# Optimization experiments

Hardware: AMD Instinct MI355X
Metric: run time of the kernel (lower is better)

Reference implementation:

```python
import jax, jax.numpy as jnp
import numpy as np
import math

D, H, L, V, F, B, S = 1024, 16, 4, 32000, 4096, 1, 2048
HD = D // H
LN_EPS = 1e-5


def _alibi_slopes(n_heads):
    # power-of-2 case from the torch code
    start = 2.0 ** (-2.0 ** (-(math.log2(n_heads) - 3)))
    return np.array([start * (start ** i) for i in range(n_heads)], dtype=np.float32)


def setup_inputs() -> dict:
    key = jax.random.key(0)
    ks = jax.random.split(key, 10)
    sc = 0.02
    return {
        "input_ids": jax.random.randint(ks[0], (B, S), 0, V, dtype=jnp.int64 if jax.config.jax_enable_x64 else jnp.int32),
        "emb": jax.random.normal(ks[1], (V, D), jnp.float32) * sc,
        "alibi_slopes": jnp.asarray(_alibi_slopes(H)),
        "Wq": jax.random.normal(ks[2], (L, D, D), jnp.float32) * sc,
        "Wk": jax.random.normal(ks[3], (L, D, D), jnp.float32) * sc,
        "Wv": jax.random.normal(ks[4], (L, D, D), jnp.float32) * sc,
        "Wo": jax.random.normal(ks[5], (L, D, D), jnp.float32) * sc,
        "W1": jax.random.normal(ks[6], (L, F, D), jnp.float32) * sc,
        "b1": jnp.zeros((L, F), jnp.float32),
        "W2": jax.random.normal(ks[7], (L, D, F), jnp.float32) * sc,
        "b2": jnp.zeros((L, D), jnp.float32),
        "g1": jnp.ones((L, D), jnp.float32),
        "beta1": jnp.zeros((L, D), jnp.float32),
        "g2": jnp.ones((L, D), jnp.float32),
        "beta2": jnp.zeros((L, D), jnp.float32),
        "gf": jnp.ones((D,), jnp.float32),
        "bf": jnp.zeros((D,), jnp.float32),
    }


def _layernorm(x, g, b):
    m = jnp.mean(x, axis=-1, keepdims=True)
    v = jnp.var(x, axis=-1, keepdims=True)
    return (x - m) * jax.lax.rsqrt(v + LN_EPS) * g + b


def _forward(input_ids, emb, alibi_slopes, Wq, Wk, Wv, Wo, W1, b1, W2, b2,
             g1, beta1, g2, beta2, gf, bf):
    x = emb[input_ids]  # [B, S, D]
    pos = jnp.arange(S, dtype=jnp.float32)
    dist = pos[None, :] - pos[:, None]          # [S, S], entry (i, j) = j - i
    causal = dist <= 0                           # tril mask
    bias = alibi_slopes[None, :, None, None] * dist  # [1, H, S, S]
    scale = 1.0 / math.sqrt(HD)

    def layer(x, p):
        wq, wk, wv, wo, w1, bb1, w2, bb2, gg1, be1, gg2, be2 = p
        h = _layernorm(x, gg1, be1)
        q = jnp.einsum('bsd,ed->bse', h, wq).reshape(B, S, H, HD).transpose(0, 2, 1, 3)
        k = jnp.einsum('bsd,ed->bse', h, wk).reshape(B, S, H, HD).transpose(0, 2, 1, 3)
        v = jnp.einsum('bsd,ed->bse', h, wv).reshape(B, S, H, HD).transpose(0, 2, 1, 3)
        scores = jnp.einsum('bhqd,bhkd->bhqk', q, k) * scale
        scores = scores - bias
        scores = jnp.where(causal, scores, -jnp.inf)
        w = jax.nn.softmax(scores, axis=-1)
        out = jnp.einsum('bhqk,bhkd->bhqd', w, v)
        out = out.transpose(0, 2, 1, 3).reshape(B, S, D)
        out = jnp.einsum('bsd,ed->bse', out, wo)
        x = x + out
        h2 = _layernorm(x, gg2, be2)
        ff = jax.nn.gelu(jnp.einsum('bsd,fd->bsf', h2, w1) + bb1, approximate=False)
        ff = jnp.einsum('bsf,df->bsd', ff, w2) + bb2
        return x + ff, None

    params = (Wq, Wk, Wv, Wo, W1, b1, W2, b2, g1, beta1, g2, beta2)
    x, _ = jax.lax.scan(layer, x, params)
    x = _layernorm(x, gf, bf)
    logits = jnp.einsum('bsd,vd->bsv', x, emb)  # tied lm_head
    return logits


def reference(input_ids, emb, alibi_slopes, Wq, Wk, Wv, Wo, W1, b1, W2, b2,
              g1, beta1, g2, beta2, gf, bf):
    return _forward(input_ids, emb, alibi_slopes, Wq, Wk, Wv, Wo, W1, b1, W2, b2,
                    g1, beta1, g2, beta2, gf, bf)
```

## Files before the change

### kernel.cpp

```cpp
#include <hip/hip_runtime.h>
#include <hip/hip_bf16.h>

typedef unsigned int u32;
typedef unsigned short u16;
typedef __attribute__((ext_vector_type(8))) __bf16 bf16x8;
typedef __attribute__((ext_vector_type(8))) unsigned short u16x8;
typedef __attribute__((ext_vector_type(4))) float f32x4;

#define SEQ 2048

__device__ __forceinline__ float b2f(u16 u) {
  union { u32 i; float f; } x; x.i = ((u32)u) << 16; return x.f;
}
__device__ __forceinline__ u16 f2b(float f) {
  u32 u = __float_as_uint(f);
  u = (u + 0x7fffu + ((u >> 16) & 1u)) >> 16;
  return (u16)u;
}
__device__ __forceinline__ void gload_lds16(const void* g, void* l) {
  __builtin_amdgcn_global_load_lds((const __attribute__((address_space(1))) u32*)g,
                                   (__attribute__((address_space(3))) u32*)l, 16, 0, 0);
}

struct CvtArgs {
  const float* src[7];
  u16* dst[7];
  u32 beg[8];
  u32 total;
};

__global__ __launch_bounds__(256) void cvt_all(CvtArgs a)
{
  for (u32 i = blockIdx.x * 256 + threadIdx.x; i < a.total; i += gridDim.x * 256) {
    int s = 0;
#pragma unroll
    for (int k = 1; k < 7; ++k) s += (i >= a.beg[k]);
    const u32 li = i - a.beg[s];
    const float* in = a.src[s];
    const float4 f0 = ((const float4*)in)[(size_t)li * 2];
    const float4 f1 = ((const float4*)in)[(size_t)li * 2 + 1];
    union { bf16x8 b; u16x8 u; } r;
    r.b[0] = (__bf16)f0.x; r.b[1] = (__bf16)f0.y;
    r.b[2] = (__bf16)f0.z; r.b[3] = (__bf16)f0.w;
    r.b[4] = (__bf16)f1.x; r.b[5] = (__bf16)f1.y;
    r.b[6] = (__bf16)f1.z; r.b[7] = (__bf16)f1.w;
    *(u16x8*)(a.dst[s] + (size_t)li * 8) = r.u;
  }
}

__global__ __launch_bounds__(512, 2) void gemm256(
    const u16* __restrict__ A, const u16* __restrict__ Bt,
    float* __restrict__ C, int N, int K)
{
  __shared__ u16 As[2][256 * 64];
  __shared__ u16 Bs[2][256 * 64];
  const int tid = threadIdx.x;
  const int lane = tid & 63;
  const int wid = tid >> 6;
  const int wr = wid >> 2;
  const int wc = wid & 3;

  const int T = (int)gridDim.x;
  const int bid = (int)blockIdx.x;
  const int q8 = T >> 3, r8 = T & 7;
  const int xcd = bid & 7, base = bid >> 3;
  const int swz = (xcd < r8 ? xcd * (q8 + 1) : r8 * (q8 + 1) + (xcd - r8) * q8) + base;
  const int m0 = (swz & 7) * 256;
  const int n0 = (swz >> 3) * 256;

  f32x4 acc[8][4] = {};

  const int srow = tid >> 3;
  const int sgr = (tid & 7) ^ (srow & 7);
  const u16* gA = A + (size_t)(m0 + srow) * K + sgr * 8;
  const u16* gB = Bt + (size_t)(n0 + srow) * K + sgr * 8;
  const int dwave = wid * 512;

  const int co0 = (((lane >> 4)) ^ (lane & 7)) * 8;
  const int co1 = (((lane >> 4) + 4) ^ (lane & 7)) * 8;
  const int raA = (wr * 128 + (lane & 15)) * 64;
  const int raB = (wc * 64 + (lane & 15)) * 64;

  const int nk = K >> 6;

#pragma unroll
  for (int c = 0; c < 4; ++c) {
    gload_lds16(gA + (size_t)(c * 64) * K, &As[0][c * 4096 + dwave]);
    gload_lds16(gB + (size_t)(c * 64) * K, &Bs[0][c * 4096 + dwave]);
  }
#pragma unroll
  for (int c = 0; c < 4; ++c) {
    gload_lds16(gA + (size_t)(c * 64) * K + 64, &As[1][c * 4096 + dwave]);
    gload_lds16(gB + (size_t)(c * 64) * K + 64, &Bs[1][c * 4096 + dwave]);
  }
  asm volatile("s_waitcnt vmcnt(8)" ::: "memory");
  __builtin_amdgcn_s_barrier();
  __builtin_amdgcn_sched_barrier(0);

#pragma unroll 2
  for (int t = 0; t < nk; ++t) {
    const int cb = t & 1;
    const u16* Acur = &As[cb][0];
    const u16* Bcur = &Bs[cb][0];

    bf16x8 bf[4][2];
#pragma unroll
    for (int n = 0; n < 4; ++n) {
      const int ro = raB + n * 16 * 64;
      bf[n][0] = *(const bf16x8*)&Bcur[ro + co0];
      bf[n][1] = *(const bf16x8*)&Bcur[ro + co1];
    }
#pragma unroll
    for (int p = 0; p < 4; ++p) {
      bf16x8 af[2][2];
#pragma unroll
      for (int mm = 0; mm < 2; ++mm) {
        const int ro = raA + (p * 32 + mm * 16) * 64;
        af[mm][0] = *(const bf16x8*)&Acur[ro + co0];
        af[mm][1] = *(const bf16x8*)&Acur[ro + co1];
      }
      __builtin_amdgcn_s_setprio(1);
#pragma unroll
      for (int mm = 0; mm < 2; ++mm)
#pragma unroll
        for (int n = 0; n < 4; ++n) {
          acc[p * 2 + mm][n] = __builtin_amdgcn_mfma_f32_16x16x32_bf16(af[mm][0], bf[n][0], acc[p * 2 + mm][n], 0, 0, 0);
          acc[p * 2 + mm][n] = __builtin_amdgcn_mfma_f32_16x16x32_bf16(af[mm][1], bf[n][1], acc[p * 2 + mm][n], 0, 0, 0);
        }
      __builtin_amdgcn_s_setprio(0);
    }

    __builtin_amdgcn_s_barrier();
    if (t + 2 < nk) {
      const size_t kto = (size_t)(t + 2) * 64;
      u16* Anx = &As[cb][0];
      u16* Bnx = &Bs[cb][0];
#pragma unroll
      for (int c = 0; c < 4; ++c) {
        gload_lds16(gA + (size_t)(c * 64) * K + kto, Anx + c * 4096 + dwave);
        gload_lds16(gB + (size_t)(c * 64) * K + kto, Bnx + c * 4096 + dwave);
      }
      asm volatile("s_waitcnt vmcnt(8)" ::: "memory");
    } else if (t + 1 < nk) {
      asm volatile("s_waitcnt vmcnt(0)" ::: "memory");
    }
    __builtin_amdgcn_s_barrier();
    __builtin_amdgcn_sched_barrier(0);
  }

  const int crow = m0 + wr * 128 + ((lane >> 4) << 2);
  const int ccol = n0 + wc * 64 + (lane & 15);
#pragma unroll
  for (int m = 0; m < 8; ++m)
#pragma unroll
    for (int n = 0; n < 4; ++n)
#pragma unroll
      for (int j = 0; j < 4; ++j)
        C[(size_t)(crow + m * 16 + j) * N + ccol + n * 16] = acc[m][n][j];
}

template <int EPI>
__global__ __launch_bounds__(256) void gemm64(
    const u16* __restrict__ A, const u16* __restrict__ B0,
    const u16* __restrict__ B1, const u16* __restrict__ B2,
    void* __restrict__ C0, void* __restrict__ C1, void* __restrict__ C2,
    const float* __restrict__ bias, int N, int K)
{
  __shared__ u16 As[64 * 64];
  __shared__ u16 Bs[128 * 64];
  const int tid = threadIdx.x;
  const int lane = tid & 63;
  const int w = tid >> 6;
  const int wr = w >> 1;
  const int wc = w & 1;

  const int T = (int)gridDim.x;
  const int bid = (int)blockIdx.x;
  const int q8 = T >> 3, r8 = T & 7;
  const int xcd = bid & 7, base = bid >> 3;
  int swz = (xcd < r8 ? xcd * (q8 + 1) : r8 * (q8 + 1) + (xcd - r8) * q8) + base;
  int which = 0;
  if (EPI == 1) which = swz >> 8;
  const u16* Bt = (which == 0) ? B0 : (which == 1) ? B1 : B2;
  const int m0 = (swz & 31) * 64;
  const int n0 = (EPI == 1 ? ((swz >> 5) & 7) : (swz >> 5)) * 128;

  const int kchunk = K / (int)gridDim.z;
  const int kbeg = (int)blockIdx.z * kchunk;
  const int kend = kbeg + kchunk;

  f32x4 acc[2][4] = {};

  const int rs = lane >> 3;
  const int gs = (lane & 7) ^ rs;
  const u16* ga0 = A + (size_t)(m0 + w * 16 + rs) * K + gs * 8;
  const u16* gb0 = Bt + (size_t)(n0 + w * 32 + rs) * K + gs * 8;
  u16* la = &As[(w * 16) * 64];
  u16* lb = &Bs[(w * 32) * 64];

  const int xg = lane & 7;
  int coff[2];
#pragma unroll
  for (int ks = 0; ks < 2; ++ks)
    coff[ks] = ((ks * 4 + (lane >> 4)) ^ xg) * 8;
  const int ra = (wr * 32 + (lane & 15)) * 64;
  const int rb = (wc * 64 + (lane & 15)) * 64;

  for (int kt = kbeg; kt < kend; kt += 64) {
    __syncthreads();
#pragma unroll
    for (int c = 0; c < 2; ++c)
      gload_lds16(ga0 + (size_t)c * 8 * K + kt, la + c * 8 * 64);
#pragma unroll
    for (int c = 0; c < 4; ++c)
      gload_lds16(gb0 + (size_t)c * 8 * K + kt, lb + c * 8 * 64);
    asm volatile("s_waitcnt vmcnt(0)" ::: "memory");
    __syncthreads();
#pragma unroll
    for (int ks = 0; ks < 2; ++ks) {
      bf16x8 af[2], bfr[4];
#pragma unroll
      for (int m = 0; m < 2; ++m)
        af[m] = *(const bf16x8*)&As[ra + m * 16 * 64 + coff[ks]];
#pragma unroll
      for (int n = 0; n < 4; ++n)
        bfr[n] = *(const bf16x8*)&Bs[rb + n * 16 * 64 + coff[ks]];
#pragma unroll
      for (int m = 0; m < 2; ++m)
#pragma unroll
        for (int n = 0; n < 4; ++n)
          acc[m][n] = __builtin_amdgcn_mfma_f32_16x16x32_bf16(af[m], bfr[n], acc[m][n], 0, 0, 0);
    }
  }

#pragma unroll
  for (int m = 0; m < 2; ++m) {
    const int rowb = m0 + wr * 32 + m * 16 + ((lane >> 4) << 2);
#pragma unroll
    for (int n = 0; n < 4; ++n) {
      const int col = n0 + wc * 64 + n * 16 + (lane & 15);
#pragma unroll
      for (int j = 0; j < 4; ++j) {
        const int r = rowb + j;
        float v = acc[m][n][j];
        if (EPI == 1) {
          u16* outp = (u16*)((which == 0) ? C0 : (which == 1) ? C1 : C2);
          outp[((size_t)(col >> 6) * SEQ + r) * 64 + (col & 63)] = f2b(v);
        } else if (EPI == 2) {
          float xx = v + bias[col];
          float ge = 0.5f * xx * (1.0f + erff(xx * 0.70710678118654752f));
          ((u16*)C0)[(size_t)r * N + col] = f2b(ge);
        } else {
          float xx = v;
          if (bias != nullptr && blockIdx.z == 0) xx += bias[col];
          atomicAdd(&((float*)C0)[(size_t)r * N + col], xx);
        }
      }
    }
  }
}

__global__ __launch_bounds__(256) void gemm_f32b(
    const u16* __restrict__ A, const float* __restrict__ Bt,
    float* __restrict__ C0, int N, int K)
{
  __shared__ u16 As[128 * 32];
  __shared__ u16 Bs[128 * 32];
  const int tid = threadIdx.x;
  const int lane = tid & 63;
  const int w = tid >> 6;
  const int wr = w >> 1;
  const int wc = w & 1;

  const int T = (int)gridDim.x;
  const int bid = (int)blockIdx.x;
  const int q8 = T >> 3, r8 = T & 7;
  const int xcd = bid & 7, base = bid >> 3;
  int swz = (xcd < r8 ? xcd * (q8 + 1) : r8 * (q8 + 1) + (xcd - r8) * q8) + base;
  const int m0 = (swz & 15) * 128;
  const int n0 = (swz >> 4) * 128;

  f32x4 acc[4][4] = {};
  const u16* ga0 = A + (size_t)(m0 + w * 32 + (lane >> 2)) * K + (lane & 3) * 8;
  u16* la = &As[(w * 32) * 32];
  const float* gb32 = Bt + (size_t)(n0 + (tid >> 1)) * K + (tid & 1) * 16;
  u16* lbw = &Bs[(tid >> 1) * 32 + (tid & 1) * 16];

  for (int kt = 0; kt < K; kt += 32) {
    __syncthreads();
    gload_lds16(ga0 + kt, la);
    gload_lds16(ga0 + kt + 16 * K, la + 16 * 32);
    {
      const float4 f0 = *(const float4*)(gb32 + kt);
      const float4 f1 = *(const float4*)(gb32 + kt + 4);
      const float4 f2 = *(const float4*)(gb32 + kt + 8);
      const float4 f3 = *(const float4*)(gb32 + kt + 12);
      union { bf16x8 b; u16x8 u; } lo, hi;
      lo.b[0] = (__bf16)f0.x; lo.b[1] = (__bf16)f0.y;
      lo.b[2] = (__bf16)f0.z; lo.b[3] = (__bf16)f0.w;
      lo.b[4] = (__bf16)f1.x; lo.b[5] = (__bf16)f1.y;
      lo.b[6] = (__bf16)f1.z; lo.b[7] = (__bf16)f1.w;
      hi.b[0] = (__bf16)f2.x; hi.b[1] = (__bf16)f2.y;
      hi.b[2] = (__bf16)f2.z; hi.b[3] = (__bf16)f2.w;
      hi.b[4] = (__bf16)f3.x; hi.b[5] = (__bf16)f3.y;
      hi.b[6] = (__bf16)f3.z; hi.b[7] = (__bf16)f3.w;
      *(u16x8*)lbw = lo.u;
      *(u16x8*)(lbw + 8) = hi.u;
    }
    asm volatile("s_waitcnt vmcnt(0)" ::: "memory");
    __syncthreads();
    bf16x8 af[4], bfr[4];
#pragma unroll
    for (int m = 0; m < 4; ++m)
      af[m] = *(const bf16x8*)&As[(wr * 64 + m * 16 + (lane & 15)) * 32 + (lane >> 4) * 8];
#pragma unroll
    for (int n = 0; n < 4; ++n)
      bfr[n] = *(const bf16x8*)&Bs[(wc * 64 + n * 16 + (lane & 15)) * 32 + (lane >> 4) * 8];
#pragma unroll
    for (int m = 0; m < 4; ++m)
#pragma unroll
      for (int n = 0; n < 4; ++n)
        acc[m][n] = __builtin_amdgcn_mfma_f32_16x16x32_bf16(af[m], bfr[n], acc[m][n], 0, 0, 0);
  }

#pragma unroll
  for (int m = 0; m < 4; ++m) {
    const int rowb = m0 + wr * 64 + m * 16 + ((lane >> 4) << 2);
#pragma unroll
    for (int n = 0; n < 4; ++n) {
      const int col = n0 + wc * 64 + n * 16 + (lane & 15);
#pragma unroll
      for (int j = 0; j < 4; ++j)
        C0[(size_t)(rowb + j) * N + col] = acc[m][n][j];
    }
  }
}

__global__ __launch_bounds__(256) void ln_kernel(const float* __restrict__ x,
    const float* __restrict__ g, const float* __restrict__ b, u16* __restrict__ out)
{
  const int row = blockIdx.x;
  const int tid = threadIdx.x;
  const float4 v = ((const float4*)(x + (size_t)row * 1024))[tid];
  float s = v.x + v.y + v.z + v.w;
  float sq = v.x * v.x + v.y * v.y + v.z * v.z + v.w * v.w;
#pragma unroll
  for (int o = 1; o < 64; o <<= 1) { s += __shfl_xor(s, o); sq += __shfl_xor(sq, o); }
  __shared__ float ss[4], ssq[4];
  if ((tid & 63) == 0) { ss[tid >> 6] = s; ssq[tid >> 6] = sq; }
  __syncthreads();
  s = ss[0] + ss[1] + ss[2] + ss[3];
  sq = ssq[0] + ssq[1] + ssq[2] + ssq[3];
  const float mean = s * (1.0f / 1024.0f);
  const float var = sq * (1.0f / 1024.0f) - mean * mean;
  const float rstd = rsqrtf(var + 1e-5f);
  const int c = tid * 4;
  u16* o4 = out + (size_t)row * 1024 + c;
  const float4 gg = ((const float4*)g)[tid];
  const float4 bb = ((const float4*)b)[tid];
  o4[0] = f2b((v.x - mean) * rstd * gg.x + bb.x);
  o4[1] = f2b((v.y - mean) * rstd * gg.y + bb.y);
  o4[2] = f2b((v.z - mean) * rstd * gg.z + bb.z);
  o4[3] = f2b((v.w - mean) * rstd * gg.w + bb.w);
}

__global__ __launch_bounds__(256) void gather_kernel(const int* __restrict__ ids,
    const float* __restrict__ emb, float* __restrict__ x)
{
  const int srow = blockIdx.x;
  const int tid = threadIdx.x;
  const int id = ids[srow];
  ((float4*)(x + (size_t)srow * 1024))[tid] =
      ((const float4*)(emb + (size_t)id * 1024))[tid];
}

__global__ __launch_bounds__(256) void attn_kernel(
    const u16* __restrict__ q, const u16* __restrict__ k, const u16* __restrict__ v,
    const float* __restrict__ slopes, u16* __restrict__ out)
{
  const int bid = (int)blockIdx.x;
  const int swz = (bid & 7) * 32 + (bid >> 3);
  const int h = swz >> 4;
  const int q0 = (swz & 15) * 128;
  const int tid = threadIdx.x;
  const int lane = tid & 63;
  const int w = tid >> 6;
  const float slope = slopes[h];

  __shared__ u16 Ks[2][64 * 32];
  __shared__ u16 Vt[64][72];
  __shared__ u16 Pl[4][32][72];

  const u16* qb = q + ((size_t)h * SEQ + q0 + w * 32) * 64;
  bf16x8 qf[2][2];
#pragma unroll
  for (int m = 0; m < 2; ++m)
#pragma unroll
    for (int kk = 0; kk < 2; ++kk)
      qf[m][kk] = *(const bf16x8*)(qb + (m * 16 + (lane & 15)) * 64 + kk * 32 + (lane >> 4) * 8);

  f32x4 o_acc[2][4] = {};
  float mrun[2][4], lrun[2][4];
#pragma unroll
  for (int m = 0; m < 2; ++m)
#pragma unroll
    for (int j = 0; j < 4; ++j) { mrun[m][j] = -1e30f; lrun[m][j] = 0.0f; }

  const int ntiles = (q0 >> 6) + 2;
  const int wmaxrow = q0 + w * 32 + 31;

  const int kkp = w >> 1, halfp = w & 1;
  const u16* gk0 = k + ((size_t)h * SEQ + halfp * 32 + (lane >> 2)) * 64 + kkp * 32 + (lane & 3) * 8;
  u16* lk = &Ks[kkp][(halfp * 32) * 32];
  const u16* gv0 = v + ((size_t)h * SEQ + lane) * 64 + w * 16;

  for (int t = 0; t < ntiles; ++t) {
    const int j0 = t << 6;
    __syncthreads();
    gload_lds16(gk0 + (size_t)j0 * 64, lk);
    gload_lds16(gk0 + (size_t)(j0 + 16) * 64, lk + 16 * 32);
    {
      const u16* gvp = gv0 + (size_t)j0 * 64;
      u16x8 v0 = *(const u16x8*)gvp;
      u16x8 v1 = *(const u16x8*)(gvp + 8);
      const int d0 = w * 16;
#pragma unroll
      for (int i = 0; i < 8; ++i) Vt[d0 + i][lane] = v0[i];
#pragma unroll
      for (int i = 0; i < 8; ++i) Vt[d0 + 8 + i][lane] = v1[i];
    }
    asm volatile("s_waitcnt vmcnt(0)" ::: "memory");
    __syncthreads();

    if (wmaxrow >= j0) {
      f32x4 s[2][4] = {};
      __builtin_amdgcn_s_setprio(1);
#pragma unroll
      for (int kk = 0; kk < 2; ++kk) {
        bf16x8 kf[4];
#pragma unroll
        for (int n = 0; n < 4; ++n)
          kf[n] = *(const bf16x8*)&Ks[kk][(n * 16 + (lane & 15)) * 32 + (lane >> 4) * 8];
#pragma unroll
        for (int m = 0; m < 2; ++m)
#pragma unroll
          for (int n = 0; n < 4; ++n)
            s[m][n] = __builtin_amdgcn_mfma_f32_16x16x32_bf16(qf[m][kk], kf[n], s[m][n], 0, 0, 0);
      }
      __builtin_amdgcn_s_setprio(0);
      const int rq = q0 + w * 32 + ((lane >> 4) << 2);
      const int ck = j0 + (lane & 15);
#pragma unroll
      for (int m = 0; m < 2; ++m) {
#pragma unroll
        for (int j = 0; j < 4; ++j) {
          const int qi = rq + m * 16 + j;
          float mx = -1e30f;
#pragma unroll
          for (int n = 0; n < 4; ++n) {
            const int kj = ck + n * 16;
            float val = s[m][n][j] * 0.125f - slope * (float)(kj - qi);
            val = (kj <= qi) ? val : -1e30f;
            s[m][n][j] = val;
            mx = fmaxf(mx, val);
          }
#pragma unroll
          for (int o = 1; o < 16; o <<= 1) mx = fmaxf(mx, __shfl_xor(mx, o));
          const float mnew = fmaxf(mrun[m][j], mx);
          const float alpha = __expf(mrun[m][j] - mnew);
          mrun[m][j] = mnew;
          float rs = 0.0f;
          const int prow = m * 16 + ((lane >> 4) << 2) + j;
#pragma unroll
          for (int n = 0; n < 4; ++n) {
            const float p = __expf(s[m][n][j] - mnew);
            rs += p;
            Pl[w][prow][n * 16 + (lane & 15)] = f2b(p);
          }
#pragma unroll
          for (int o = 1; o < 16; o <<= 1) rs += __shfl_xor(rs, o);
          lrun[m][j] = lrun[m][j] * alpha + rs;
#pragma unroll
          for (int n = 0; n < 4; ++n) o_acc[m][n][j] *= alpha;
        }
      }
      __builtin_amdgcn_s_setprio(1);
#pragma unroll
      for (int kk = 0; kk < 2; ++kk) {
        bf16x8 pf[2], vf[4];
#pragma unroll
        for (int m = 0; m < 2; ++m)
          pf[m] = *(const bf16x8*)&Pl[w][m * 16 + (lane & 15)][kk * 32 + (lane >> 4) * 8];
#pragma unroll
        for (int n = 0; n < 4; ++n)
          vf[n] = *(const bf16x8*)&Vt[n * 16 + (lane & 15)][kk * 32 + (lane >> 4) * 8];
#pragma unroll
        for (int m = 0; m < 2; ++m)
#pragma unroll
          for (int n = 0; n < 4; ++n)
            o_acc[m][n] = __builtin_amdgcn_mfma_f32_16x16x32_bf16(pf[m], vf[n], o_acc[m][n], 0, 0, 0);
      }
      __builtin_amdgcn_s_setprio(0);
    }
  }

#pragma unroll
  for (int m = 0; m < 2; ++m) {
    const int sbase = q0 + w * 32 + m * 16 + ((lane >> 4) << 2);
#pragma unroll
    for (int n = 0; n < 4; ++n) {
      const int d = h * 64 + n * 16 + (lane & 15);
#pragma unroll
      for (int j = 0; j < 4; ++j)
        out[(size_t)(sbase + j) * 1024 + d] = f2b(o_acc[m][n][j] / lrun[m][j]);
    }
  }
}

extern "C" void kernel_launch(void* const* d_in, const int* in_sizes, int n_in,
                              void* d_out, int out_size, void* d_ws, size_t ws_size,
                              hipStream_t stream)
{
  (void)in_sizes; (void)n_in; (void)out_size;
  const int* ids = (const int*)d_in[0];
  const float* emb = (const float*)d_in[1];
  const float* slopes = (const float*)d_in[2];
  const float* Wq = (const float*)d_in[3];
  const float* Wk = (const float*)d_in[4];
  const float* Wv = (const float*)d_in[5];
  const float* Wo = (const float*)d_in[6];
  const float* W1 = (const float*)d_in[7];
  const float* b1 = (const float*)d_in[8];
  const float* W2 = (const float*)d_in[9];
  const float* b2 = (const float*)d_in[10];
  const float* g1 = (const float*)d_in[11];
  const float* be1 = (const float*)d_in[12];
  const float* g2 = (const float*)d_in[13];
  const float* be2 = (const float*)d_in[14];
  const float* gf = (const float*)d_in[15];
  const float* bfin = (const float*)d_in[16];

  char* ob = (char*)d_out;
  float* x   = (float*)ob;
  u16* qb    = (u16*)(ob + (size_t)( 8u << 20));
  u16* kb    = (u16*)(ob + (size_t)(12u << 20));
  u16* vb    = (u16*)(ob + (size_t)(16u << 20));
  u16* attn  = (u16*)(ob + (size_t)(20u << 20));
  u16* ff    = (u16*)(ob + (size_t)(24u << 20));
  u16* Wq_b  = (u16*)(ob + (size_t)( 40u << 20));
  u16* Wk_b  = (u16*)(ob + (size_t)( 48u << 20));
  u16* Wv_b  = (u16*)(ob + (size_t)( 56u << 20));
  u16* Wo_b  = (u16*)(ob + (size_t)( 64u << 20));
  u16* W1_b  = (u16*)(ob + (size_t)( 72u << 20));
  u16* W2_b  = (u16*)(ob + (size_t)(104u << 20));
  u16* h     = (u16*)d_ws;
  const size_t emb_b_need = (size_t)(4u << 20) + (size_t)32000 * 1024 * 2;
  const bool emb_fits = ws_size >= emb_b_need;
  u16* emb_b = (u16*)((char*)d_ws + (4u << 20));
  float* logits = (float*)d_out;

  {
    CvtArgs a;
    const u32 wsz = 4 * 1024 * 1024 / 8;
    const u32 fsz = 16 * 1024 * 1024 / 8;
    const u32 esz = 32000 * 1024 / 8;
    a.src[0] = Wq; a.dst[0] = Wq_b;
    a.src[1] = Wk; a.dst[1] = Wk_b;
    a.src[2] = Wv; a.dst[2] = Wv_b;
    a.src[3] = Wo; a.dst[3] = Wo_b;
    a.src[4] = W1; a.dst[4] = W1_b;
    a.src[5] = W2; a.dst[5] = W2_b;
    a.src[6] = emb; a.dst[6] = emb_b;
    a.beg[0] = 0;
    a.beg[1] = wsz;      a.beg[2] = 2 * wsz;  a.beg[3] = 3 * wsz;
    a.beg[4] = 4 * wsz;  a.beg[5] = 4 * wsz + fsz;  a.beg[6] = 4 * wsz + 2 * fsz;
    a.beg[7] = a.beg[6] + esz;
    a.total = emb_fits ? a.beg[7] : a.beg[6];
    cvt_all<<<2048, 256, 0, stream>>>(a);
  }

  gather_kernel<<<2048, 256, 0, stream>>>(ids, emb, x);

  for (int l = 0; l < 4; ++l) {
    const size_t wo = (size_t)l * 1024 * 1024;
    const size_t wf = (size_t)l * 4096 * 1024;
    ln_kernel<<<2048, 256, 0, stream>>>(x, g1 + l * 1024, be1 + l * 1024, h);
    gemm64<1><<<dim3(768, 1, 1), 256, 0, stream>>>(h, Wq_b + wo, Wk_b + wo, Wv_b + wo,
        qb, kb, vb, nullptr, 1024, 1024);
    attn_kernel<<<dim3(256, 1, 1), 256, 0, stream>>>(qb, kb, vb, slopes, attn);
    gemm64<3><<<dim3(256, 1, 2), 256, 0, stream>>>(attn, Wo_b + wo, nullptr, nullptr,
        x, nullptr, nullptr, nullptr, 1024, 1024);
    ln_kernel<<<2048, 256, 0, stream>>>(x, g2 + l * 1024, be2 + l * 1024, h);
    gemm64<2><<<dim3(1024, 1, 1), 256, 0, stream>>>(h, W1_b + wf, nullptr, nullptr,
        ff, nullptr, nullptr, b1 + l * 4096, 4096, 1024);
    gemm64<3><<<dim3(256, 1, 2), 256, 0, stream>>>(ff, W2_b + wf, nullptr, nullptr,
        x, nullptr, nullptr, b2 + l * 1024, 1024, 4096);
  }
  ln_kernel<<<2048, 256, 0, stream>>>(x, gf, bfin, h);
  if (emb_fits) {
    gemm256<<<dim3(1000, 1, 1), 512, 0, stream>>>(h, emb_b, logits, 32000, 1024);
  } else {
    gemm_f32b<<<dim3(4000, 1, 1), 256, 0, stream>>>(h, emb, logits, 32000, 1024);
  }
}
```

Measured before the change: 1.319 ms.

## Replace gemm64 with double-buffered 128x128 GEMM, fuse QKV weights and residual+LN

Replaces the single-buffered 64x128 GEMM with a 128x128 tile kernel that double-buffers LDS loads and raises MFMA priority. The Q/K/V weights are interleaved per layer at conversion time so one N=3072 GEMM produces all three projections. Split-K partial sums now go to two fp32 scratch buffers instead of atomics, and a new ln_res kernel adds residual, partials and bias and then applies the next LayerNorm. This removes the atomics and the separate LN launches, at the cost of extra scratch traffic and fewer blocks for the N=1024 GEMMs.

```diff
diff --git a/kernel.cpp b/kernel.cpp
--- a/kernel.cpp
+++ b/kernel.cpp
@@ -44,7 +44,15 @@
     r.b[2] = (__bf16)f0.z; r.b[3] = (__bf16)f0.w;
     r.b[4] = (__bf16)f1.x; r.b[5] = (__bf16)f1.y;
     r.b[6] = (__bf16)f1.z; r.b[7] = (__bf16)f1.w;
-    *(u16x8*)(a.dst[s] + (size_t)li * 8) = r.u;
+    u16* d;
+    if (s < 3) {
+      const u32 layer = li >> 17;
+      const u32 rem = li & 131071u;
+      d = a.dst[s] + ((size_t)layer * 393216u + rem) * 8;
+    } else {
+      d = a.dst[s] + (size_t)li * 8;
+    }
+    *(u16x8*)d = r.u;
   }
 }
 
@@ -160,82 +168,110 @@
 }
 
 template <int EPI>
-__global__ __launch_bounds__(256) void gemm64(
-    const u16* __restrict__ A, const u16* __restrict__ B0,
-    const u16* __restrict__ B1, const u16* __restrict__ B2,
+__global__ __launch_bounds__(256, 2) void gemm128p(
+    const u16* __restrict__ A, const u16* __restrict__ Bt,
     void* __restrict__ C0, void* __restrict__ C1, void* __restrict__ C2,
     const float* __restrict__ bias, int N, int K)
 {
-  __shared__ u16 As[64 * 64];
-  __shared__ u16 Bs[128 * 64];
+  __shared__ u16 As[2][128 * 64];
+  __shared__ u16 Bs[2][128 * 64];
   const int tid = threadIdx.x;
   const int lane = tid & 63;
-  const int w = tid >> 6;
-  const int wr = w >> 1;
-  const int wc = w & 1;
+  const int wid = tid >> 6;
+  const int wr = wid >> 1;
+  const int wc = wid & 1;
 
   const int T = (int)gridDim.x;
   const int bid = (int)blockIdx.x;
   const int q8 = T >> 3, r8 = T & 7;
   const int xcd = bid & 7, base = bid >> 3;
-  int swz = (xcd < r8 ? xcd * (q8 + 1) : r8 * (q8 + 1) + (xcd - r8) * q8) + base;
-  int which = 0;
-  if (EPI == 1) which = swz >> 8;
-  const u16* Bt = (which == 0) ? B0 : (which == 1) ? B1 : B2;
-  const int m0 = (swz & 31) * 64;
-  const int n0 = (EPI == 1 ? ((swz >> 5) & 7) : (swz >> 5)) * 128;
+  const int swz = (xcd < r8 ? xcd * (q8 + 1) : r8 * (q8 + 1) + (xcd - r8) * q8) + base;
+  const int m0 = (swz & 15) * 128;
+  const int n0 = (swz >> 4) * 128;
 
   const int kchunk = K / (int)gridDim.z;
   const int kbeg = (int)blockIdx.z * kchunk;
-  const int kend = kbeg + kchunk;
-
-  f32x4 acc[2][4] = {};
-
-  const int rs = lane >> 3;
-  const int gs = (lane & 7) ^ rs;
-  const u16* ga0 = A + (size_t)(m0 + w * 16 + rs) * K + gs * 8;
-  const u16* gb0 = Bt + (size_t)(n0 + w * 32 + rs) * K + gs * 8;
-  u16* la = &As[(w * 16) * 64];
-  u16* lb = &Bs[(w * 32) * 64];
-
-  const int xg = lane & 7;
-  int coff[2];
-#pragma unroll
-  for (int ks = 0; ks < 2; ++ks)
-    coff[ks] = ((ks * 4 + (lane >> 4)) ^ xg) * 8;
-  const int ra = (wr * 32 + (lane & 15)) * 64;
-  const int rb = (wc * 64 + (lane & 15)) * 64;
-
-  for (int kt = kbeg; kt < kend; kt += 64) {
-    __syncthreads();
-#pragma unroll
-    for (int c = 0; c < 2; ++c)
-      gload_lds16(ga0 + (size_t)c * 8 * K + kt, la + c * 8 * 64);
-#pragma unroll
-    for (int c = 0; c < 4; ++c)
-      gload_lds16(gb0 + (size_t)c * 8 * K + kt, lb + c * 8 * 64);
-    asm volatile("s_waitcnt vmcnt(0)" ::: "memory");
-    __syncthreads();
-#pragma unroll
-    for (int ks = 0; ks < 2; ++ks) {
-      bf16x8 af[2], bfr[4];
-#pragma unroll
-      for (int m = 0; m < 2; ++m)
-        af[m] = *(const bf16x8*)&As[ra + m * 16 * 64 + coff[ks]];
-#pragma unroll
-      for (int n = 0; n < 4; ++n)
-        bfr[n] = *(const bf16x8*)&Bs[rb + n * 16 * 64 + coff[ks]];
-#pragma unroll
-      for (int m = 0; m < 2; ++m)
-#pragma unroll
-        for (int n = 0; n < 4; ++n)
-          acc[m][n] = __builtin_amdgcn_mfma_f32_16x16x32_bf16(af[m], bfr[n], acc[m][n], 0, 0, 0);
-    }
-  }
-
-#pragma unroll
-  for (int m = 0; m < 2; ++m) {
-    const int rowb = m0 + wr * 32 + m * 16 + ((lane >> 4) << 2);
+  const int nk = kchunk >> 6;
+
+  f32x4 acc[4][4] = {};
+
+  const int srow = tid >> 3;
+  const int sgr = (tid & 7) ^ (srow & 7);
+  const u16* gA = A + (size_t)(m0 + srow) * K + kbeg + sgr * 8;
+  const u16* gB = Bt + (size_t)(n0 + srow) * K + kbeg + sgr * 8;
+  const int dwave = wid * 512;
+
+  const int co0 = (((lane >> 4)) ^ (lane & 7)) * 8;
+  const int co1 = (((lane >> 4) + 4) ^ (lane & 7)) * 8;
+  const int raA = (wr * 64 + (lane & 15)) * 64;
+  const int raB = (wc * 64 + (lane & 15)) * 64;
+
+#pragma unroll
+  for (int c = 0; c < 4; ++c) {
+    gload_lds16(gA + (size_t)(c * 32) * K, &As[0][c * 2048 + dwave]);
+    gload_lds16(gB + (size_t)(c * 32) * K, &Bs[0][c * 2048 + dwave]);
+  }
+#pragma unroll
+  for (int c = 0; c < 4; ++c) {
+    gload_lds16(gA + (size_t)(c * 32) * K + 64, &As[1][c * 2048 + dwave]);
+    gload_lds16(gB + (size_t)(c * 32) * K + 64, &Bs[1][c * 2048 + dwave]);
+  }
+  asm volatile("s_waitcnt vmcnt(8)" ::: "memory");
+  __builtin_amdgcn_s_barrier();
+  __builtin_amdgcn_sched_barrier(0);
+
+#pragma unroll 2
+  for (int t = 0; t < nk; ++t) {
+    const int cb = t & 1;
+    const u16* Acur = &As[cb][0];
+    const u16* Bcur = &Bs[cb][0];
+
+    bf16x8 bf[4][2];
+#pragma unroll
+    for (int n = 0; n < 4; ++n) {
+      const int ro = raB + n * 16 * 64;
+      bf[n][0] = *(const bf16x8*)&Bcur[ro + co0];
+      bf[n][1] = *(const bf16x8*)&Bcur[ro + co1];
+    }
+#pragma unroll
+    for (int p = 0; p < 4; ++p) {
+      bf16x8 af[2];
+      {
+        const int ro = raA + p * 16 * 64;
+        af[0] = *(const bf16x8*)&Acur[ro + co0];
+        af[1] = *(const bf16x8*)&Acur[ro + co1];
+      }
+      __builtin_amdgcn_s_setprio(1);
+#pragma unroll
+      for (int n = 0; n < 4; ++n) {
+        acc[p][n] = __builtin_amdgcn_mfma_f32_16x16x32_bf16(af[0], bf[n][0], acc[p][n], 0, 0, 0);
+        acc[p][n] = __builtin_amdgcn_mfma_f32_16x16x32_bf16(af[1], bf[n][1], acc[p][n], 0, 0, 0);
+      }
+      __builtin_amdgcn_s_setprio(0);
+    }
+
+    __builtin_amdgcn_s_barrier();
+    if (t + 2 < nk) {
+      const size_t kto = (size_t)(t + 2) * 64;
+      u16* Anx = &As[cb][0];
+      u16* Bnx = &Bs[cb][0];
+#pragma unroll
+      for (int c = 0; c < 4; ++c) {
+        gload_lds16(gA + (size_t)(c * 32) * K + kto, Anx + c * 2048 + dwave);
+        gload_lds16(gB + (size_t)(c * 32) * K + kto, Bnx + c * 2048 + dwave);
+      }
+      asm volatile("s_waitcnt vmcnt(8)" ::: "memory");
+    } else if (t + 1 < nk) {
+      asm volatile("s_waitcnt vmcnt(0)" ::: "memory");
+    }
+    __builtin_amdgcn_s_barrier();
+    __builtin_amdgcn_sched_barrier(0);
+  }
+
+  const int z = (int)blockIdx.z;
+#pragma unroll
+  for (int m = 0; m < 4; ++m) {
+    const int rowb = m0 + wr * 64 + m * 16 + ((lane >> 4) << 2);
 #pragma unroll
     for (int n = 0; n < 4; ++n) {
       const int col = n0 + wc * 64 + n * 16 + (lane & 15);
@@ -243,17 +279,18 @@
       for (int j = 0; j < 4; ++j) {
         const int r = rowb + j;
         float v = acc[m][n][j];
-        if (EPI == 1) {
+        if (EPI == 0) {
+          float* outp = (float*)(z == 0 ? C0 : C1);
+          outp[(size_t)r * N + col] = v;
+        } else if (EPI == 1) {
+          const int which = col >> 10;
+          const int ci = col & 1023;
           u16* outp = (u16*)((which == 0) ? C0 : (which == 1) ? C1 : C2);
-          outp[((size_t)(col >> 6) * SEQ + r) * 64 + (col & 63)] = f2b(v);
-        } else if (EPI == 2) {
+          outp[((size_t)(ci >> 6) * SEQ + r) * 64 + (ci & 63)] = f2b(v);
+        } else {
           float xx = v + bias[col];
           float ge = 0.5f * xx * (1.0f + erff(xx * 0.70710678118654752f));
           ((u16*)C0)[(size_t)r * N + col] = f2b(ge);
-        } else {
-          float xx = v;
-          if (bias != nullptr && blockIdx.z == 0) xx += bias[col];
-          atomicAdd(&((float*)C0)[(size_t)r * N + col], xx);
         }
       }
     }
@@ -364,6 +401,47 @@
   o4[3] = f2b((v.w - mean) * rstd * gg.w + bb.w);
 }
 
+__global__ __launch_bounds__(256) void ln_res(float* __restrict__ x,
+    const float* __restrict__ p0, const float* __restrict__ p1,
+    const float* __restrict__ bias,
+    const float* __restrict__ g, const float* __restrict__ b,
+    u16* __restrict__ out)
+{
+  const int row = blockIdx.x;
+  const int tid = threadIdx.x;
+  const size_t off = (size_t)row * 1024;
+  float4 v = ((const float4*)(x + off))[tid];
+  const float4 a0 = ((const float4*)(p0 + off))[tid];
+  const float4 a1 = ((const float4*)(p1 + off))[tid];
+  v.x += a0.x + a1.x; v.y += a0.y + a1.y;
+  v.z += a0.z + a1.z; v.w += a0.w + a1.w;
+  if (bias != nullptr) {
+    const float4 bi = ((const float4*)bias)[tid];
+    v.x += bi.x; v.y += bi.y; v.z += bi.z; v.w += bi.w;
+  }
+  ((float4*)(x + off))[tid] = v;
+  float s = v.x + v.y + v.z + v.w;
+  float sq = v.x * v.x + v.y * v.y + v.z * v.z + v.w * v.w;
+#pragma unroll
+  for (int o = 1; o < 64; o <<= 1) { s += __shfl_xor(s, o); sq += __shfl_xor(sq, o); }
+  __shared__ float ss[4], ssq[4];
+  if ((tid & 63) == 0) { ss[tid >> 6] = s; ssq[tid >> 6] = sq; }
+  __syncthreads();
+  s = ss[0] + ss[1] + ss[2] + ss[3];
+  sq = ssq[0] + ssq[1] + ssq[2] + ssq[3];
+  const float mean = s * (1.0f / 1024.0f);
+  const float var = sq * (1.0f / 1024.0f) - mean * mean;
+  const float rstd = rsqrtf(var + 1e-5f);
+  const int c = tid * 4;
+  u16* o4 = out + off + c;
+  const float4 gg = ((const float4*)g)[tid];
+  const float4 bb = ((const float4*)b)[tid];
+  o4[0] = f2b((v.x - mean) * rstd * gg.x + bb.x);
+  o4[1] = f2b((v.y - mean) * rstd * gg.y + bb.y);
+  o4[2] = f2b((v.z - mean) * rstd * gg.z + bb.z);
+  o4[3] = f2b((v.w - mean) * rstd * gg.w + bb.w);
+}
+
 __global__ __launch_bounds__(256) void gather_kernel(const int* __restrict__ ids,
     const float* __restrict__ emb, float* __restrict__ x)
 {
@@ -541,19 +619,19 @@
   const float* bfin = (const float*)d_in[16];
 
   char* ob = (char*)d_out;
-  float* x   = (float*)ob;
-  u16* qb    = (u16*)(ob + (size_t)( 8u << 20));
-  u16* kb    = (u16*)(ob + (size_t)(12u << 20));
-  u16* vb    = (u16*)(ob + (size_t)(16u << 20));
-  u16* attn  = (u16*)(ob + (size_t)(20u << 20));
-  u16* ff    = (u16*)(ob + (size_t)(24u << 20));
-  u16* Wq_b  = (u16*)(ob + (size_t)( 40u << 20));
-  u16* Wk_b  = (u16*)(ob + (size_t)( 48u << 20));
-  u16* Wv_b  = (u16*)(ob + (size_t)( 56u << 20));
-  u16* Wo_b  = (u16*)(ob + (size_t)( 64u << 20));
-  u16* W1_b  = (u16*)(ob + (size_t)( 72u << 20));
-  u16* W2_b  = (u16*)(ob + (size_t)(104u << 20));
-  u16* h     = (u16*)d_ws;
+  float* x    = (float*)ob;
+  u16* qb     = (u16*)(ob + (size_t)( 8u << 20));
+  u16* kb     = (u16*)(ob + (size_t)(12u << 20));
+  u16* vb     = (u16*)(ob + (size_t)(16u << 20));
+  u16* attn   = (u16*)(ob + (size_t)(20u << 20));
+  u16* ff     = (u16*)(ob + (size_t)(24u << 20));
+  u16* Wqkv_b = (u16*)(ob + (size_t)( 40u << 20));
+  u16* Wo_b   = (u16*)(ob + (size_t)( 64u << 20));
+  u16* W1_b   = (u16*)(ob + (size_t)( 72u << 20));
+  u16* W2_b   = (u16*)(ob + (size_t)(104u << 20));
+  float* p0   = (float*)(ob + (size_t)(136u << 20));
+  float* p1   = (float*)(ob + (size_t)(144u << 20));
+  u16* h      = (u16*)d_ws;
   const size_t emb_b_need = (size_t)(4u << 20) + (size_t)32000 * 1024 * 2;
   const bool emb_fits = ws_size >= emb_b_need;
   u16* emb_b = (u16*)((char*)d_ws + (4u << 20));
@@ -564,9 +642,9 @@
     const u32 wsz = 4 * 1024 * 1024 / 8;
     const u32 fsz = 16 * 1024 * 1024 / 8;
     const u32 esz = 32000 * 1024 / 8;
-    a.src[0] = Wq; a.dst[0] = Wq_b;
-    a.src[1] = Wk; a.dst[1] = Wk_b;
-    a.src[2] = Wv; a.dst[2] = Wv_b;
+    a.src[0] = Wq; a.dst[0] = Wqkv_b;
+    a.src[1] = Wk; a.dst[1] = Wqkv_b + 1024 * 1024;
+    a.src[2] = Wv; a.dst[2] = Wqkv_b + 2 * 1024 * 1024;
     a.src[3] = Wo; a.dst[3] = Wo_b;
     a.src[4] = W1; a.dst[4] = W1_b;
     a.src[5] = W2; a.dst[5] = W2_b;
@@ -580,23 +658,31 @@
   }
 
   gather_kernel<<<2048, 256, 0, stream>>>(ids, emb, x);
+  ln_kernel<<<2048, 256, 0, stream>>>(x, g1, be1, h);
 
   for (int l = 0; l < 4; ++l) {
+    const size_t wqkv = (size_t)l * 3072 * 1024;
     const size_t wo = (size_t)l * 1024 * 1024;
     const size_t wf = (size_t)l * 4096 * 1024;
-    ln_kernel<<<2048, 256, 0, stream>>>(x, g1 + l * 1024, be1 + l * 1024, h);
-    gemm64<1><<<dim3(768, 1, 1), 256, 0, stream>>>(h, Wq_b + wo, Wk_b + wo, Wv_b + wo,
-        qb, kb, vb, nullptr, 1024, 1024);
+    gemm128p<1><<<dim3(384, 1, 1), 256, 0, stream>>>(h, Wqkv_b + wqkv,
+        qb, kb, vb, nullptr, 3072, 1024);
     attn_kernel<<<dim3(256, 1, 1), 256, 0, stream>>>(qb, kb, vb, slopes, attn);
-    gemm64<3><<<dim3(256, 1, 2), 256, 0, stream>>>(attn, Wo_b + wo, nullptr, nullptr,
-        x, nullptr, nullptr, nullptr, 1024, 1024);
-    ln_kernel<<<2048, 256, 0, stream>>>(x, g2 + l * 1024, be2 + l * 1024, h);
-    gemm64<2><<<dim3(1024, 1, 1), 256, 0, stream>>>(h, W1_b + wf, nullptr, nullptr,
+    gemm128p<0><<<dim3(128, 1, 2), 256, 0, stream>>>(attn, Wo_b + wo,
+        p0, p1, nullptr, nullptr, 1024, 1024);
+    ln_res<<<2048, 256, 0, stream>>>(x, p0, p1, nullptr,
+        g2 + l * 1024, be2 + l * 1024, h);
+    gemm128p<2><<<dim3(512, 1, 1), 256, 0, stream>>>(h, W1_b + wf,
         ff, nullptr, nullptr, b1 + l * 4096, 4096, 1024);
-    gemm64<3><<<dim3(256, 1, 2), 256, 0, stream>>>(ff, W2_b + wf, nullptr, nullptr,
-        x, nullptr, nullptr, b2 + l * 1024, 1024, 4096);
-  }
-  ln_kernel<<<2048, 256, 0, stream>>>(x, gf, bfin, h);
+    gemm128p<0><<<dim3(128, 1, 2), 256, 0, stream>>>(ff, W2_b + wf,
+        p0, p1, nullptr, nullptr, 1024, 4096);
+    if (l < 3) {
+      ln_res<<<2048, 256, 0, stream>>>(x, p0, p1, b2 + l * 1024,
+          g1 + (l + 1) * 1024, be1 + (l + 1) * 1024, h);
+    } else {
+      ln_res<<<2048, 256, 0, stream>>>(x, p0, p1, b2 + l * 1024, gf, bfin, h);
+    }
+  }
+
   if (emb_fits) {
     gemm256<<<dim3(1000, 1, 1), 512, 0, stream>>>(h, emb_b, logits, 32000, 1024);
   } else {
```

After: 1.287 ms. 2.4% less time.
